# Optimization experiments

Hardware: AMD Instinct MI355X
Metric: run time of the kernel (lower is better)

Reference implementation:

```python
import jax, jax.numpy as jnp
import numpy as np

H = 16        # heads
DH = 64       # dim_head
DM = 1024     # query_dim = context_dim
INNER = H * DH


def setup_inputs() -> dict:
    key = jax.random.key(0)
    ks = jax.random.split(key, 5)
    s = 0.02
    queries = jax.random.normal(ks[0], (2, 2048, DM), dtype=jnp.float32)
    Wq = jax.random.normal(ks[1], (DM, INNER), dtype=jnp.float32) * s
    Wkv = jax.random.normal(ks[2], (DM, 2 * INNER), dtype=jnp.float32) * s
    Wo = jax.random.normal(ks[3], (INNER, DM), dtype=jnp.float32) * s
    bo = jax.random.normal(ks[4], (DM,), dtype=jnp.float32) * s
    return {"queries": queries, "Wq": Wq, "Wkv": Wkv, "Wo": Wo, "bo": bo}


def reference(queries, Wq, Wkv, Wo, bo):
    b, n, _ = queries.shape
    scale = DH ** -0.5
    q = queries @ Wq                       # [b, n, inner]
    kv = queries @ Wkv                     # self-attention: context = queries
    k, v = jnp.split(kv, 2, axis=-1)
    # b n (h d) -> b h n d
    split_heads = lambda t: t.reshape(b, n, H, DH).transpose(0, 2, 1, 3)
    q, k, v = map(split_heads, (q, k, v))
    sim = jnp.einsum('bhid,bhjd->bhij', q, k) * scale
    attn = jax.nn.softmax(sim, axis=-1)    # dropout is identity (p=0 / eval)
    out = jnp.einsum('bhij,bhjd->bhid', attn, v)
    out = out.transpose(0, 2, 1, 3).reshape(b, n, INNER)
    return out @ Wo + bo
```

## Files before the change

### kernel.cpp

```cpp
#include <hip/hip_runtime.h>
#include <math.h>
#include <stdint.h>

typedef _Float16 half8v __attribute__((ext_vector_type(8)));
typedef _Float16 half4v __attribute__((ext_vector_type(4)));
typedef _Float16 half2v __attribute__((ext_vector_type(2)));
typedef __fp16 fp16x2 __attribute__((ext_vector_type(2)));
typedef float floatx4 __attribute__((ext_vector_type(4)));

#define MFMA16(a, b, c) __builtin_amdgcn_mfma_f32_16x16x32_f16(a, b, c, 0, 0, 0)

#define QSCALE 0.18033688011112f

__device__ __forceinline__ void gld_lds16(const void* g, void* l) {
  __builtin_amdgcn_global_load_lds(
      (const __attribute__((address_space(1))) uint32_t*)(uintptr_t)g,
      (__attribute__((address_space(3))) uint32_t*)(uintptr_t)l, 16, 0, 0);
}

__device__ __forceinline__ half2v pk16(float a, float b) {
  fp16x2 t = __builtin_amdgcn_cvt_pkrtz(a, b);
  return __builtin_bit_cast(half2v, t);
}

__device__ __forceinline__ int swz(int row, int blk) {
  return row * 64 + ((blk ^ (row & 7)) << 3);
}

__device__ __forceinline__ int vswz(int row, int blk) {
  return row * 32 + ((blk ^ ((row >> 1) & 3)) << 3);
}

__device__ __forceinline__ int gswz(int row, int blk) {
  return row * 32 + ((blk ^ ((row >> 1) & 3)) << 3);
}

__global__ __launch_bounds__(256) void prep(
    const float* __restrict__ X, const float* __restrict__ Wq,
    const float* __restrict__ Wkv, const float* __restrict__ Wo,
    _Float16* __restrict__ X16, _Float16* __restrict__ WqkvT,
    _Float16* __restrict__ WoT)
{
  __shared__ alignas(16) _Float16 Tt[64 * 68];
  const int bid = blockIdx.x;
  if (bid < 2048) {
    size_t gid = (size_t)bid * 256 + threadIdx.x;
    const float4* src = (const float4*)(X) + gid * 2;
    float4 a = src[0], b = src[1];
    half8v h;
    h[0]=(_Float16)a.x; h[1]=(_Float16)a.y; h[2]=(_Float16)a.z; h[3]=(_Float16)a.w;
    h[4]=(_Float16)b.x; h[5]=(_Float16)b.y; h[6]=(_Float16)b.z; h[7]=(_Float16)b.w;
    *((half8v*)X16 + gid) = h;
    return;
  }
  int b = bid - 2048;
  const float* src; _Float16* dst; int N, tk, tn;
  if (b < 256)      { src = Wq;  dst = WqkvT;                 N = 1024; tk = b & 15;        tn = b >> 4; }
  else if (b < 768) { src = Wkv; dst = WqkvT + (size_t)1024 * 1024; N = 2048; tk = (b - 256) & 15; tn = (b - 256) >> 4; }
  else              { src = Wo;  dst = WoT;                   N = 1024; tk = (b - 768) & 15; tn = (b - 768) >> 4; }

  const int t = threadIdx.x;
  {
    int kg = t >> 4, ng = t & 15;
    const float* sp = src + (size_t)(tk * 64 + kg * 4) * N + tn * 64 + ng * 4;
    float4 r0 = *(const float4*)(sp);
    float4 r1 = *(const float4*)(sp + N);
    float4 r2 = *(const float4*)(sp + 2 * N);
    float4 r3 = *(const float4*)(sp + 3 * N);
    half4v h;
    h[0]=(_Float16)r0.x; h[1]=(_Float16)r1.x; h[2]=(_Float16)r2.x; h[3]=(_Float16)r3.x;
    *(half4v*)&Tt[(ng * 4 + 0) * 68 + kg * 4] = h;
    h[0]=(_Float16)r0.y; h[1]=(_Float16)r1.y; h[2]=(_Float16)r2.y; h[3]=(_Float16)r3.y;
    *(half4v*)&Tt[(ng * 4 + 1) * 68 + kg * 4] = h;
    h[0]=(_Float16)r0.z; h[1]=(_Float16)r1.z; h[2]=(_Float16)r2.z; h[3]=(_Float16)r3.z;
    *(half4v*)&Tt[(ng * 4 + 2) * 68 + kg * 4] = h;
    h[0]=(_Float16)r0.w; h[1]=(_Float16)r1.w; h[2]=(_Float16)r2.w; h[3]=(_Float16)r3.w;
    *(half4v*)&Tt[(ng * 4 + 3) * 68 + kg * 4] = h;
  }
  __syncthreads();
  #pragma unroll
  for (int i = 0; i < 2; i++) {
    int idx = t + i * 256;
    int nl = idx >> 3, k8 = (idx & 7) * 8;
    half8v v = *(half8v*)&Tt[nl * 68 + k8];
    *(half8v*)(dst + (size_t)(tn * 64 + nl) * 1024 + tk * 64 + k8) = v;
  }
}

__global__ __launch_bounds__(256) void qkv_gemm(
    const _Float16* __restrict__ X16, const _Float16* __restrict__ WqkvT,
    _Float16* __restrict__ q_ws, _Float16* __restrict__ k_ws,
    _Float16* __restrict__ vT_ws)
{
  constexpr int K = 1024;
  __shared__ alignas(16) _Float16 Tt[128 * 136];
  _Float16* As = Tt;
  _Float16* Bs = Tt + 4096;

  const int m0 = blockIdx.x * 128;
  const int n0 = blockIdx.y * 128;

  const int tid  = threadIdx.x;
  const int wave = tid >> 6, lane = tid & 63;
  const int qd = lane >> 4, l15 = lane & 15;
  const int wr = (wave >> 1) * 64, wc = (wave & 1) * 64;
  const int r0i = tid >> 2;
  const int cbs = (((tid & 3) ^ ((r0i >> 1) & 3))) * 8;

  floatx4 acc[4][4] = {};

  for (int k0 = 0; k0 < K; k0 += 32) {
    gld_lds16(X16 + (size_t)(m0 + r0i) * K + k0 + cbs, &As[tid * 8]);
    gld_lds16(X16 + (size_t)(m0 + 64 + r0i) * K + k0 + cbs, &As[(tid + 256) * 8]);
    gld_lds16(WqkvT + (size_t)(n0 + r0i) * K + k0 + cbs, &Bs[tid * 8]);
    gld_lds16(WqkvT + (size_t)(n0 + 64 + r0i) * K + k0 + cbs, &Bs[(tid + 256) * 8]);
    __syncthreads();
    half8v a[4], b[4];
    #pragma unroll
    for (int it = 0; it < 4; it++)
      a[it] = *(half8v*)&As[gswz(wr + it * 16 + l15, qd)];
    #pragma unroll
    for (int jt = 0; jt < 4; jt++)
      b[jt] = *(half8v*)&Bs[gswz(wc + jt * 16 + l15, qd)];
    #pragma unroll
    for (int it = 0; it < 4; it++)
      #pragma unroll
      for (int jt = 0; jt < 4; jt++)
        acc[it][jt] = MFMA16(a[it], b[jt], acc[it][jt]);
    __syncthreads();
  }

  if (n0 < 2048) {
    #pragma unroll
    for (int it = 0; it < 4; it++) {
      #pragma unroll
      for (int jt = 0; jt < 4; jt++) {
        #pragma unroll
        for (int r = 0; r < 4; r++) {
          int m = m0 + wr + it * 16 + qd * 4 + r;
          int n = n0 + wc + jt * 16 + l15;
          float val = acc[it][jt][r];
          int bb = m >> 11, nn = m & 2047;
          if (n0 < 1024) {
            int h = n >> 6, d = n & 63;
            q_ws[(((size_t)bb * 16 + h) * 2048 + nn) * 64 + d] = (_Float16)(val * QSCALE);
          } else {
            int c = n - 1024, h = c >> 6, d = c & 63;
            k_ws[(((size_t)bb * 16 + h) * 2048 + nn) * 64 + d] = (_Float16)val;
          }
        }
      }
    }
  } else {
    #pragma unroll
    for (int it = 0; it < 4; it++) {
      #pragma unroll
      for (int jt = 0; jt < 4; jt++) {
        #pragma unroll
        for (int r = 0; r < 4; r++) {
          int ml = wr + it * 16 + qd * 4 + r;
          int nl = wc + jt * 16 + l15;
          Tt[nl * 136 + ml] = (_Float16)acc[it][jt][r];
        }
      }
    }
    __syncthreads();
    int row = tid >> 1;
    int mh  = (tid & 1) * 64;
    int c   = (n0 - 2048) + row;
    int bb  = m0 >> 11;
    int nnb = (m0 & 2047) + mh;
    _Float16* dstp =
        vT_ws + (((size_t)bb * 16 + (c >> 6)) * 64 + (c & 63)) * 2048 + nnb;
    #pragma unroll
    for (int i = 0; i < 8; i++)
      *(half8v*)(dstp + i * 8) = *(half8v*)&Tt[row * 136 + mh + i * 8];
  }
}

__global__ __launch_bounds__(128, 2) void attn_kernel(
    const _Float16* __restrict__ q_ws, const _Float16* __restrict__ k_ws,
    const _Float16* __restrict__ vT_ws, _Float16* __restrict__ aout)
{
  constexpr int N = 2048;
  __shared__ alignas(16) _Float16 Qs[64 * 64];
  __shared__ alignas(16) _Float16 Ks[2][32 * 64];
  __shared__ alignas(16) _Float16 Vts[2][64 * 32];

  const int id = blockIdx.x;
  const int bh = ((id >> 8) << 3) | (id & 7);
  const int qt = (id >> 3) & 31;

  const _Float16* Qp = q_ws + (size_t)bh * N * 64;
  const _Float16* Kp = k_ws + (size_t)bh * N * 64;
  const _Float16* Vp = vT_ws + (size_t)bh * 64 * N;

  const int tid = threadIdx.x, wave = tid >> 6, lane = tid & 63;
  const int qd = lane >> 4, l15 = lane & 15;
  const int q0 = qt * 64;
  const int wbase = wave * 32;

  #pragma unroll
  for (int i = 0; i < 4; i++) {
    int idx = tid + i * 128;
    int r = idx >> 3, cb = (idx ^ r) & 7;
    gld_lds16(Qp + (size_t)(q0 + r) * 64 + cb * 8, &Qs[idx * 8]);
  }
  #pragma unroll
  for (int i = 0; i < 2; i++) {
    int idx = tid + i * 128;
    { int r = idx >> 3, cb = (idx ^ r) & 7;
      gld_lds16(Kp + (size_t)r * 64 + cb * 8, &Ks[0][idx * 8]); }
    { int r = idx >> 2, cb = ((idx & 3) ^ ((r >> 1) & 3));
      gld_lds16(Vp + (size_t)r * N + cb * 8, &Vts[0][idx * 8]); }
  }
  __syncthreads();

  half8v qf[2][2];
  #pragma unroll
  for (int m = 0; m < 2; m++)
    #pragma unroll
    for (int ks = 0; ks < 2; ks++)
      qf[m][ks] = *(half8v*)&Qs[swz(wbase + m * 16 + l15, ks * 4 + qd)];

  floatx4 o[2][4] = {};
  float lsum[2] = {};

  int p = 0;
  for (int kv0 = 0; kv0 < N; kv0 += 32) {
    const bool more = (kv0 + 32) < N;
    if (more) {
      int kvn = kv0 + 32;
      #pragma unroll
      for (int i = 0; i < 2; i++) {
        int idx = tid + i * 128;
        { int r = idx >> 3, cb = (idx ^ r) & 7;
          gld_lds16(Kp + (size_t)(kvn + r) * 64 + cb * 8,
                    &Ks[p ^ 1][idx * 8]); }
        { int r = idx >> 2, cb = ((idx & 3) ^ ((r >> 1) & 3));
          gld_lds16(Vp + (size_t)r * N + kvn + cb * 8,
                    &Vts[p ^ 1][idx * 8]); }
      }
    }

    floatx4 s[2][2] = {};
    #pragma unroll
    for (int ks = 0; ks < 2; ks++) {
      half8v kf[2];
      #pragma unroll
      for (int nt = 0; nt < 2; nt++)
        kf[nt] = *(half8v*)&Ks[p][swz(nt * 16 + l15, ks * 4 + qd)];
      #pragma unroll
      for (int nt = 0; nt < 2; nt++)
        #pragma unroll
        for (int m = 0; m < 2; m++)
          s[nt][m] = MFMA16(kf[nt], qf[m][ks], s[nt][m]);
    }

    #pragma unroll
    for (int m = 0; m < 2; m++) {
      #pragma unroll
      for (int nt = 0; nt < 2; nt++) {
        float p0 = __builtin_amdgcn_exp2f(s[nt][m][0]);
        float p1 = __builtin_amdgcn_exp2f(s[nt][m][1]);
        float p2 = __builtin_amdgcn_exp2f(s[nt][m][2]);
        float p3 = __builtin_amdgcn_exp2f(s[nt][m][3]);
        lsum[m] += (p0 + p1) + (p2 + p3);
        half2v h01 = pk16(p0, p1);
        half2v h23 = pk16(p2, p3);
        half4v pk;
        pk[0] = h01[0]; pk[1] = h01[1]; pk[2] = h23[0]; pk[3] = h23[1];
        *(half4v*)&Qs[swz(wbase + m * 16 + l15, 2 * nt + (qd >> 1)) +
                      (qd & 1) * 4] = pk;
      }
    }

    {
      half8v pf[2], vf[4];
      #pragma unroll
      for (int m = 0; m < 2; m++)
        pf[m] = *(half8v*)&Qs[swz(wbase + m * 16 + l15, qd)];
      #pragma unroll
      for (int dt = 0; dt < 4; dt++)
        vf[dt] = *(half8v*)&Vts[p][vswz(dt * 16 + l15, qd)];
      #pragma unroll
      for (int m = 0; m < 2; m++)
        #pragma unroll
        for (int dt = 0; dt < 4; dt++)
          o[m][dt] = MFMA16(pf[m], vf[dt], o[m][dt]);
    }

    if (more) __syncthreads();
    p ^= 1;
  }

  #pragma unroll
  for (int m = 0; m < 2; m++) {
    lsum[m] += __shfl_xor(lsum[m], 16);
    lsum[m] += __shfl_xor(lsum[m], 32);
  }

  const int bb = bh >> 4, hh = bh & 15;
  #pragma unroll
  for (int m = 0; m < 2; m++) {
    #pragma unroll
    for (int r = 0; r < 4; r++) {
      float inv = 1.0f / __shfl(lsum[m], qd * 4 + r);
      int n = q0 + wbase + m * 16 + qd * 4 + r;
      #pragma unroll
      for (int dt = 0; dt < 4; dt++) {
        int d = dt * 16 + l15;
        aout[((size_t)(bb * 2048 + n)) * 1024 + hh * 64 + d] =
            (_Float16)(o[m][dt][r] * inv);
      }
    }
  }
}

__global__ __launch_bounds__(256) void out_gemm(
    const _Float16* __restrict__ A, const _Float16* __restrict__ WoT,
    const float* __restrict__ bo, float* __restrict__ Out)
{
  constexpr int K = 1024;
  __shared__ alignas(16) _Float16 As[64 * 32];
  __shared__ alignas(16) _Float16 Bs[128 * 32];

  const int m0 = blockIdx.x * 64;
  const int n0 = blockIdx.y * 128;
  const int tid = threadIdx.x;
  const int wave = tid >> 6, lane = tid & 63;
  const int qd = lane >> 4, l15 = lane & 15;
  const int wr = (wave >> 1) * 32, wc = (wave & 1) * 64;
  const int r0i = tid >> 2;
  const int cbs = (((tid & 3) ^ ((r0i >> 1) & 3))) * 8;

  floatx4 acc[2][4] = {};

  for (int k0 = 0; k0 < K; k0 += 32) {
    gld_lds16(A + (size_t)(m0 + r0i) * K + k0 + cbs, &As[tid * 8]);
    gld_lds16(WoT + (size_t)(n0 + r0i) * K + k0 + cbs, &Bs[tid * 8]);
    gld_lds16(WoT + (size_t)(n0 + 64 + r0i) * K + k0 + cbs, &Bs[(tid + 256) * 8]);
    __syncthreads();
    half8v a[2], b[4];
    #pragma unroll
    for (int it = 0; it < 2; it++)
      a[it] = *(half8v*)&As[gswz(wr + it * 16 + l15, qd)];
    #pragma unroll
    for (int jt = 0; jt < 4; jt++)
      b[jt] = *(half8v*)&Bs[gswz(wc + jt * 16 + l15, qd)];
    #pragma unroll
    for (int it = 0; it < 2; it++)
      #pragma unroll
      for (int jt = 0; jt < 4; jt++)
        acc[it][jt] = MFMA16(a[it], b[jt], acc[it][jt]);
    __syncthreads();
  }

  #pragma unroll
  for (int it = 0; it < 2; it++) {
    #pragma unroll
    for (int jt = 0; jt < 4; jt++) {
      int n = n0 + wc + jt * 16 + l15;
      float bias = bo[n];
      #pragma unroll
      for (int r = 0; r < 4; r++) {
        int m = m0 + wr + it * 16 + qd * 4 + r;
        Out[(size_t)m * 1024 + n] = acc[it][jt][r] + bias;
      }
    }
  }
}

extern "C" void kernel_launch(void* const* d_in, const int* in_sizes, int n_in,
                              void* d_out, int out_size, void* d_ws, size_t ws_size,
                              hipStream_t stream) {
  const float* X   = (const float*)d_in[0];
  const float* Wq  = (const float*)d_in[1];
  const float* Wkv = (const float*)d_in[2];
  const float* Wo  = (const float*)d_in[3];
  const float* bo  = (const float*)d_in[4];
  float* out = (float*)d_out;

  const size_t M4 = (size_t)4 * 1024 * 1024;
  _Float16* q_ws   = (_Float16*)d_ws;
  _Float16* k_ws   = q_ws + M4;
  _Float16* vT_ws  = k_ws + M4;
  _Float16* X16    = vT_ws + M4;
  _Float16* WqkvT  = X16 + M4;
  _Float16* WoT    = WqkvT + (size_t)3 * 1024 * 1024;
  _Float16* aout   = X16;

  prep<<<3072, 256, 0, stream>>>(X, Wq, Wkv, Wo, X16, WqkvT, WoT);
  qkv_gemm<<<dim3(32, 24), 256, 0, stream>>>(X16, WqkvT, q_ws, k_ws, vT_ws);
  attn_kernel<<<1024, 128, 0, stream>>>(q_ws, k_ws, vT_ws, aout);
  out_gemm<<<dim3(64, 8), 256, 0, stream>>>(aout, WoT, bo, out);
}
```

Measured before the change: 191.5 us.

## Split KV range across waves and load K/V directly from global into registers

The attention kernel now uses 256 threads, with two wave pairs splitting the KV sequence. Each wave streams its own 32-key slice directly from global memory into registers instead of staging K/V through double-buffered LDS. This removes the per-iteration barriers. Partial outputs and row sums from the two KV halves are reduced through shared memory at the end, and each row is written with vectorised half8 stores. MFMA sections are wrapped in setprio hints. The change risks higher global load latency exposure and uncoalesced V-transpose reads in exchange for more parallelism and no synchronisation.

```diff
diff --git a/kernel.cpp b/kernel.cpp
--- a/kernel.cpp
+++ b/kernel.cpp
@@ -178,14 +178,14 @@
   }
 }
 
-__global__ __launch_bounds__(128, 2) void attn_kernel(
+__global__ __launch_bounds__(256, 4) void attn_kernel(
     const _Float16* __restrict__ q_ws, const _Float16* __restrict__ k_ws,
     const _Float16* __restrict__ vT_ws, _Float16* __restrict__ aout)
 {
   constexpr int N = 2048;
-  __shared__ alignas(16) _Float16 Qs[64 * 64];
-  __shared__ alignas(16) _Float16 Ks[2][32 * 64];
-  __shared__ alignas(16) _Float16 Vts[2][64 * 32];
+  __shared__ alignas(16) char smem[35328];
+  _Float16* Pbase = (_Float16*)smem;
+  _Float16* Qs    = (_Float16*)(smem + 8192);
 
   const int id = blockIdx.x;
   const int bh = ((id >> 8) << 3) | (id & 7);
@@ -198,22 +198,16 @@
   const int tid = threadIdx.x, wave = tid >> 6, lane = tid & 63;
   const int qd = lane >> 4, l15 = lane & 15;
   const int q0 = qt * 64;
-  const int wbase = wave * 32;
-
-  #pragma unroll
-  for (int i = 0; i < 4; i++) {
-    int idx = tid + i * 128;
+  const int qw = wave >> 1, kw = wave & 1;
+
+  _Float16* Ps = Pbase + wave * 1024;
+
+  #pragma unroll
+  for (int i = 0; i < 2; i++) {
+    int idx = tid + i * 256;
     int r = idx >> 3, cb = (idx ^ r) & 7;
     gld_lds16(Qp + (size_t)(q0 + r) * 64 + cb * 8, &Qs[idx * 8]);
   }
-  #pragma unroll
-  for (int i = 0; i < 2; i++) {
-    int idx = tid + i * 128;
-    { int r = idx >> 3, cb = (idx ^ r) & 7;
-      gld_lds16(Kp + (size_t)r * 64 + cb * 8, &Ks[0][idx * 8]); }
-    { int r = idx >> 2, cb = ((idx & 3) ^ ((r >> 1) & 3));
-      gld_lds16(Vp + (size_t)r * N + cb * 8, &Vts[0][idx * 8]); }
-  }
   __syncthreads();
 
   half8v qf[2][2];
@@ -221,44 +215,43 @@
   for (int m = 0; m < 2; m++)
     #pragma unroll
     for (int ks = 0; ks < 2; ks++)
-      qf[m][ks] = *(half8v*)&Qs[swz(wbase + m * 16 + l15, ks * 4 + qd)];
+      qf[m][ks] = *(half8v*)&Qs[swz(qw * 32 + m * 16 + l15, ks * 4 + qd)];
+
+  const _Float16* Kw = Kp + (size_t)kw * 32 * 64;
+  const _Float16* Vw = Vp + kw * 32;
 
   floatx4 o[2][4] = {};
-  float lsum[2] = {};
-
-  int p = 0;
-  for (int kv0 = 0; kv0 < N; kv0 += 32) {
-    const bool more = (kv0 + 32) < N;
-    if (more) {
-      int kvn = kv0 + 32;
-      #pragma unroll
-      for (int i = 0; i < 2; i++) {
-        int idx = tid + i * 128;
-        { int r = idx >> 3, cb = (idx ^ r) & 7;
-          gld_lds16(Kp + (size_t)(kvn + r) * 64 + cb * 8,
-                    &Ks[p ^ 1][idx * 8]); }
-        { int r = idx >> 2, cb = ((idx & 3) ^ ((r >> 1) & 3));
-          gld_lds16(Vp + (size_t)r * N + kvn + cb * 8,
-                    &Vts[p ^ 1][idx * 8]); }
-      }
-    }
+  float lsum[2] = {0.f, 0.f};
+
+  #pragma unroll 2
+  for (int i = 0; i < 32; ++i) {
+    const size_t kvg = (size_t)i * 64;
+
+    half8v kf[2][2];
+    #pragma unroll
+    for (int ks = 0; ks < 2; ks++)
+      #pragma unroll
+      for (int nt = 0; nt < 2; nt++)
+        kf[ks][nt] = *(const half8v*)(Kw + (kvg + nt * 16 + l15) * 64 +
+                                      (ks * 4 + qd) * 8);
+    half8v vf[4];
+    #pragma unroll
+    for (int dt = 0; dt < 4; dt++)
+      vf[dt] = *(const half8v*)(Vw + (size_t)(dt * 16 + l15) * N + kvg + qd * 8);
 
     floatx4 s[2][2] = {};
-    #pragma unroll
-    for (int ks = 0; ks < 2; ks++) {
-      half8v kf[2];
-      #pragma unroll
-      for (int nt = 0; nt < 2; nt++)
-        kf[nt] = *(half8v*)&Ks[p][swz(nt * 16 + l15, ks * 4 + qd)];
+    __builtin_amdgcn_s_setprio(1);
+    #pragma unroll
+    for (int ks = 0; ks < 2; ks++)
       #pragma unroll
       for (int nt = 0; nt < 2; nt++)
         #pragma unroll
         for (int m = 0; m < 2; m++)
-          s[nt][m] = MFMA16(kf[nt], qf[m][ks], s[nt][m]);
-    }
-
-    #pragma unroll
-    for (int m = 0; m < 2; m++) {
+          s[nt][m] = MFMA16(kf[ks][nt], qf[m][ks], s[nt][m]);
+    __builtin_amdgcn_s_setprio(0);
+
+    #pragma unroll
+    for (int m = 0; m < 2; m++)
       #pragma unroll
       for (int nt = 0; nt < 2; nt++) {
         float p0 = __builtin_amdgcn_exp2f(s[nt][m][0]);
@@ -270,28 +263,20 @@
         half2v h23 = pk16(p2, p3);
         half4v pk;
         pk[0] = h01[0]; pk[1] = h01[1]; pk[2] = h23[0]; pk[3] = h23[1];
-        *(half4v*)&Qs[swz(wbase + m * 16 + l15, 2 * nt + (qd >> 1)) +
-                      (qd & 1) * 4] = pk;
+        *(half4v*)&Ps[vswz(m * 16 + l15, 2 * nt + (qd >> 1)) + (qd & 1) * 4] = pk;
       }
-    }
-
-    {
-      half8v pf[2], vf[4];
-      #pragma unroll
-      for (int m = 0; m < 2; m++)
-        pf[m] = *(half8v*)&Qs[swz(wbase + m * 16 + l15, qd)];
+
+    half8v pf[2];
+    #pragma unroll
+    for (int m = 0; m < 2; m++)
+      pf[m] = *(half8v*)&Ps[vswz(m * 16 + l15, qd)];
+    __builtin_amdgcn_s_setprio(1);
+    #pragma unroll
+    for (int m = 0; m < 2; m++)
       #pragma unroll
       for (int dt = 0; dt < 4; dt++)
-        vf[dt] = *(half8v*)&Vts[p][vswz(dt * 16 + l15, qd)];
-      #pragma unroll
-      for (int m = 0; m < 2; m++)
-        #pragma unroll
-        for (int dt = 0; dt < 4; dt++)
-          o[m][dt] = MFMA16(pf[m], vf[dt], o[m][dt]);
-    }
-
-    if (more) __syncthreads();
-    p ^= 1;
+        o[m][dt] = MFMA16(pf[m], vf[dt], o[m][dt]);
+    __builtin_amdgcn_s_setprio(0);
   }
 
   #pragma unroll
@@ -300,21 +285,42 @@
     lsum[m] += __shfl_xor(lsum[m], 32);
   }
 
+  __syncthreads();
+  float* sc = (float*)smem;
+  float* ls = (float*)(smem + 34816);
+  float* my = sc + wave * 2176;
+  #pragma unroll
+  for (int m = 0; m < 2; m++) {
+    #pragma unroll
+    for (int dt = 0; dt < 4; dt++)
+      #pragma unroll
+      for (int r = 0; r < 4; r++)
+        my[(m * 16 + qd * 4 + r) * 68 + dt * 16 + l15] = o[m][dt][r];
+    if (qd == 0) ls[wave * 32 + m * 16 + l15] = lsum[m];
+  }
+  __syncthreads();
+
   const int bb = bh >> 4, hh = bh & 15;
-  #pragma unroll
-  for (int m = 0; m < 2; m++) {
-    #pragma unroll
-    for (int r = 0; r < 4; r++) {
-      float inv = 1.0f / __shfl(lsum[m], qd * 4 + r);
-      int n = q0 + wbase + m * 16 + qd * 4 + r;
-      #pragma unroll
-      for (int dt = 0; dt < 4; dt++) {
-        int d = dt * 16 + l15;
-        aout[((size_t)(bb * 2048 + n)) * 1024 + hh * 64 + d] =
-            (_Float16)(o[m][dt][r] * inv);
-      }
-    }
-  }
+  const int row = tid >> 2, c0 = (tid & 3) * 16;
+  const int qw2 = row >> 5, r32 = row & 31;
+  const float* sa = sc + (qw2 * 2 + 0) * 2176 + r32 * 68 + c0;
+  const float* sb = sc + (qw2 * 2 + 1) * 2176 + r32 * 68 + c0;
+  float lsv = ls[(qw2 * 2 + 0) * 32 + r32] + ls[(qw2 * 2 + 1) * 32 + r32];
+  float inv = 1.0f / lsv;
+  _Float16 hv[16];
+  #pragma unroll
+  for (int j = 0; j < 4; j++) {
+    floatx4 a = *(const floatx4*)(sa + j * 4);
+    floatx4 b = *(const floatx4*)(sb + j * 4);
+    floatx4 sum = a + b;
+    half2v h01 = pk16(sum[0] * inv, sum[1] * inv);
+    half2v h23 = pk16(sum[2] * inv, sum[3] * inv);
+    hv[j * 4 + 0] = h01[0]; hv[j * 4 + 1] = h01[1];
+    hv[j * 4 + 2] = h23[0]; hv[j * 4 + 3] = h23[1];
+  }
+  _Float16* dst = aout + ((size_t)(bb * 2048 + q0 + row)) * 1024 + hh * 64 + c0;
+  *(half8v*)(dst)     = *(half8v*)&hv[0];
+  *(half8v*)(dst + 8) = *(half8v*)&hv[8];
 }
 
 __global__ __launch_bounds__(256) void out_gemm(
@@ -392,6 +398,6 @@
 
   prep<<<3072, 256, 0, stream>>>(X, Wq, Wkv, Wo, X16, WqkvT, WoT);
   qkv_gemm<<<dim3(32, 24), 256, 0, stream>>>(X16, WqkvT, q_ws, k_ws, vT_ws);
-  attn_kernel<<<1024, 128, 0, stream>>>(q_ws, k_ws, vT_ws, aout);
+  attn_kernel<<<1024, 256, 0, stream>>>(q_ws, k_ws, vT_ws, aout);
   out_gemm<<<dim3(64, 8), 256, 0, stream>>>(aout, WoT, bo, out);
 }
```

Measured after the change: 248.9 us. 30.0% more time.
